# Kernel optimization log

Hardware: AMD Instinct MI355X
Metric: run time of the kernel (lower is better)

## Reference

```python
import jax, jax.numpy as jnp
import numpy as np
from jax.ops import segment_sum

N_NODES = 100000
N_EDGES = 3200000
NUM_FEATURES = 256


def setup_inputs() -> dict:
    key = jax.random.key(0)
    ks = jax.random.split(key, 12)
    def lin(k, fan_in, fan_out):
        bound = 1.0 / np.sqrt(fan_in)
        kw, kb = jax.random.split(k)
        W = jax.random.uniform(kw, (fan_in, fan_out), jnp.float32, -bound, bound)
        b = jax.random.uniform(kb, (fan_out,), jnp.float32, -bound, bound)
        return W, b
    x = jax.random.normal(ks[0], (N_NODES, NUM_FEATURES), jnp.float32)
    edge_index = jax.random.randint(ks[1], (2, N_EDGES), 0, N_NODES, jnp.int64 if jax.config.jax_enable_x64 else jnp.int32)
    W1, b1 = lin(ks[2], NUM_FEATURES, 64)
    W2, b2 = lin(ks[3], 64, 32)
    W3, b3 = lin(ks[4], 32, 16)
    Ws02, bs02 = lin(ks[5], NUM_FEATURES, 32)
    Ws03, bs03 = lin(ks[6], NUM_FEATURES, 16)
    Ws13, bs13 = lin(ks[7], 64, 16)
    Wout, bout = lin(ks[8], 16, 1)
    return dict(x=x, edge_index=edge_index, W1=W1, b1=b1, W2=W2, b2=b2,
                W3=W3, b3=b3, Ws02=Ws02, bs02=bs02, Ws03=Ws03, bs03=bs03,
                Ws13=Ws13, bs13=bs13, Wout=Wout, bout=bout)


def _deg_inv_sqrt(edge_index, n_nodes):
    # gcn_norm with self-loops: degree counted at target nodes, +1 for self-loop
    dst = edge_index[1]
    deg = segment_sum(jnp.ones(edge_index.shape[1], jnp.float32), dst, num_segments=n_nodes) + 1.0
    return jnp.where(deg > 0, jax.lax.rsqrt(deg), 0.0)


def _gcn_conv(x, W, b, edge_index, dinv):
    # PyG GCNConv: h = x W; out[i] = sum_{j->i} dinv[j]*dinv[i]*h[j] + dinv[i]^2*h[i] + b
    src, dst = edge_index[0], edge_index[1]
    h = x @ W                                   # [N, out]
    norm = (dinv[src] * dinv[dst])[:, None]     # [E, 1]
    agg = segment_sum(h[src] * norm, dst, num_segments=x.shape[0])
    agg = agg + (dinv * dinv)[:, None] * h      # self-loop term
    return agg + b


def reference(x, edge_index, W1, b1, W2, b2, W3, b3,
              Ws02, bs02, Ws03, bs03, Ws13, bs13, Wout, bout):
    # Dropout in eval mode (identity).
    dinv = _deg_inv_sqrt(edge_index, x.shape[0])
    x1 = jax.nn.relu(_gcn_conv(x, W1, b1, edge_index, dinv))
    x2 = jax.nn.relu(_gcn_conv(x1, W2, b2, edge_index, dinv) + x @ Ws02 + bs02)
    x3 = jax.nn.relu(_gcn_conv(x2, W3, b3, edge_index, dinv)
                     + x @ Ws03 + bs03 + x1 @ Ws13 + bs13)
    return jax.nn.sigmoid(x3 @ Wout + bout)
```

## Files before the change

kernel.cpp:

```cpp
#include <hip/hip_runtime.h>
#include <hip/hip_bf16.h>
#include <math.h>


#define NBUCK_MAX 512
#define P1_CHUNK 8192
#define EPT 32
#define BCAP 9216

typedef __attribute__((ext_vector_type(8))) short bfrag;
typedef __attribute__((ext_vector_type(4))) float f4_t;

__device__ inline float uaf(unsigned u) { return __uint_as_float(u); }
__device__ inline ushort f2bf(float f) {
    __hip_bfloat16 b = __float2bfloat16(f);
    return *reinterpret_cast<ushort*>(&b);
}
__device__ inline bfrag cvt8(const float4 a, const float4 b) {
    union { ushort u[8]; bfrag f; } r;
    r.u[0] = f2bf(a.x); r.u[1] = f2bf(a.y); r.u[2] = f2bf(a.z); r.u[3] = f2bf(a.w);
    r.u[4] = f2bf(b.x); r.u[5] = f2bf(b.y); r.u[6] = f2bf(b.z); r.u[7] = f2bf(b.w);
    return r.f;
}
__device__ inline bfrag ld_bfrag(const ushort* p) {
    const uint4 raw = *reinterpret_cast<const uint4*>(p);
    return *reinterpret_cast<const bfrag*>(&raw);
}


__global__ __launch_bounds__(256) void bucket_hist_kernel(
    const int* __restrict__ dst, int E, int* __restrict__ bucket_count, int nbuckets)
{
    __shared__ int lhist[NBUCK_MAX];
    for (int i = threadIdx.x; i < nbuckets; i += 256) lhist[i] = 0;
    __syncthreads();
    const int stride = gridDim.x * 256;
    for (int e = blockIdx.x * 256 + threadIdx.x; e < E; e += stride)
        atomicAdd(&lhist[dst[e] >> 8], 1);
    __syncthreads();
    for (int i = threadIdx.x; i < nbuckets; i += 256) {
        int c = lhist[i];
        if (c) atomicAdd(&bucket_count[i], c);
    }
}

__global__ __launch_bounds__(512) void bucket_scan_kernel(
    const int* __restrict__ bucket_count, int* __restrict__ bucket_base,
    int* __restrict__ bucket_cursor, int nbuckets)
{
    __shared__ int tmp[512];
    const int tid = threadIdx.x;
    int v = (tid < nbuckets) ? bucket_count[tid] : 0;
    tmp[tid] = v;
    __syncthreads();
    for (int off = 1; off < 512; off <<= 1) {
        int t = (tid >= off) ? tmp[tid - off] : 0;
        __syncthreads();
        tmp[tid] += t;
        __syncthreads();
    }
    if (tid < nbuckets) {
        int base = tmp[tid] - v;
        bucket_base[tid]   = base;
        bucket_cursor[tid] = base;
    }
}

__global__ __launch_bounds__(256) void partition_kernel(
    const int* __restrict__ src, const int* __restrict__ dst, int E,
    int* __restrict__ bucket_cursor, unsigned int* __restrict__ keys, int nbuckets)
{
    __shared__ int hist[NBUCK_MAX];
    __shared__ int lofs[NBUCK_MAX];
    __shared__ int gbase[NBUCK_MAX];
    __shared__ int lcur[NBUCK_MAX];
    __shared__ int ssum[256];
    __shared__ unsigned int stage[P1_CHUNK];
    __shared__ int gidx[P1_CHUNK];

    const int tid = threadIdx.x;
    const int e0  = blockIdx.x * P1_CHUNK;
    const int nE  = min(P1_CHUNK, E - e0);

    for (int i = tid; i < NBUCK_MAX; i += 256) { hist[i] = 0; lcur[i] = 0; }
    __syncthreads();

    int myb[EPT];
    unsigned int mypk[EPT];
#pragma unroll
    for (int j = 0; j < EPT; ++j) {
        const int e = e0 + tid + j * 256;
        if (e < E) {
            const int d = dst[e];
            myb[j]  = d >> 8;
            mypk[j] = ((unsigned int)(d & 255) << 17) | (unsigned int)src[e];
            atomicAdd(&hist[myb[j]], 1);
        } else myb[j] = -1;
    }
    __syncthreads();

    int a0 = (2 * tid     < nbuckets) ? hist[2 * tid]     : 0;
    int a1 = (2 * tid + 1 < nbuckets) ? hist[2 * tid + 1] : 0;
    ssum[tid] = a0 + a1;
    __syncthreads();
    for (int off = 1; off < 256; off <<= 1) {
        int t = (tid >= off) ? ssum[tid - off] : 0;
        __syncthreads();
        ssum[tid] += t;
        __syncthreads();
    }
    const int ex = ssum[tid] - (a0 + a1);
    if (2 * tid     < nbuckets) lofs[2 * tid]     = ex;
    if (2 * tid + 1 < nbuckets) lofs[2 * tid + 1] = ex + a0;
    __syncthreads();

    for (int i = tid; i < nbuckets; i += 256)
        gbase[i] = atomicAdd(&bucket_cursor[i], hist[i]);
    __syncthreads();

#pragma unroll
    for (int j = 0; j < EPT; ++j) {
        if (myb[j] >= 0) {
            const int b = myb[j];
            const int l = lofs[b] + atomicAdd(&lcur[b], 1);
            stage[l] = mypk[j];
            gidx[l]  = gbase[b] - lofs[b] + l;
        }
    }
    __syncthreads();

    for (int i = tid; i < nE; i += 256)
        keys[gidx[i]] = stage[i];
}

__global__ __launch_bounds__(256) void csr_build_kernel(
    const unsigned int* __restrict__ keys, const int* __restrict__ bucket_base,
    const int* __restrict__ bucket_count,
    int* __restrict__ row_off, float* __restrict__ dinv, int* __restrict__ col,
    int N, int E)
{
    __shared__ unsigned int inb[BCAP];
    __shared__ int outv[BCAP];
    __shared__ int hist[256];
    __shared__ int lofs[256];
    __shared__ int ssum[256];

    const int tid  = threadIdx.x;
    const int b    = blockIdx.x;
    const int base = bucket_base[b];
    const int cnt  = min(bucket_count[b], BCAP);
    const int n0   = b << 8;
    const int nn   = min(256, N - n0);

    for (int i = tid; i < cnt; i += 256) inb[i] = keys[base + i];
    hist[tid] = 0;
    __syncthreads();

    for (int i = tid; i < cnt; i += 256)
        atomicAdd(&hist[inb[i] >> 17], 1);
    __syncthreads();

    ssum[tid] = hist[tid];
    __syncthreads();
    for (int off = 1; off < 256; off <<= 1) {
        int t = (tid >= off) ? ssum[tid - off] : 0;
        __syncthreads();
        ssum[tid] += t;
        __syncthreads();
    }
    lofs[tid] = ssum[tid] - hist[tid];

    if (tid < nn) {
        row_off[n0 + tid] = base + lofs[tid];
        dinv[n0 + tid]    = rsqrtf((float)hist[tid] + 1.0f);
    }
    if (b == 0 && tid == 0) row_off[N] = E;
    __syncthreads();

    hist[tid] = 0;
    __syncthreads();

    for (int i = tid; i < cnt; i += 256) {
        const unsigned int k = inb[i];
        const int node = k >> 17;
        const int l = lofs[node] + atomicAdd(&hist[node], 1);
        outv[l] = (int)(k & 0x1FFFF);
    }
    __syncthreads();

    for (int i = tid; i < cnt; i += 256)
        col[base + i] = outv[i];
}


__global__ __launch_bounds__(256) void prep_weights_kernel(
    const float* __restrict__ W1, const float* __restrict__ Ws02,
    const float* __restrict__ Ws03, const float* __restrict__ W2,
    const float* __restrict__ Ws13, const float* __restrict__ W3,
    ushort* __restrict__ Wt0, ushort* __restrict__ Wt1, ushort* __restrict__ Wt2)
{
    int idx = blockIdx.x * 256 + threadIdx.x;
    if (idx < 32768) {
        int f = idx >> 8, k = idx & 255;
        float v = 0.f;
        if (f < 64)       v = W1[k * 64 + f];
        else if (f < 96)  v = Ws02[k * 32 + (f - 64)];
        else if (f < 112) v = Ws03[k * 16 + (f - 96)];
        Wt0[idx] = f2bf(v);
    } else if (idx < 32768 + 3072) {
        int t = idx - 32768;
        int f = t >> 6, k = t & 63;
        float v = (f < 32) ? W2[k * 32 + f] : Ws13[k * 16 + (f - 32)];
        Wt1[t] = f2bf(v);
    } else if (idx < 32768 + 3072 + 512) {
        int t = idx - 32768 - 3072;
        int f = t >> 5, k = t & 31;
        Wt2[t] = f2bf(W3[k * 16 + f]);
    }
}


__global__ __launch_bounds__(256, 2) void gemm_mfma0(
    const float* __restrict__ X, const ushort* __restrict__ Wt0,
    const float* __restrict__ bs02, const float* __restrict__ bs03,
    const float* __restrict__ dinv,
    __hip_bfloat16* __restrict__ g1, float* __restrict__ pre2,
    float* __restrict__ pre3, int N)
{
    __shared__ __align__(16) float Xs[64 * 256];

    const int tid  = threadIdx.x;
    const int lane = tid & 63;
    const int wf   = tid >> 6;
    const int n0   = blockIdx.x * 64;
    const int mrow = lane & 15;
    const int kq   = (lane >> 4) * 8;

    bfrag bfr[2][8];
#pragma unroll
    for (int ft = 0; ft < 2; ++ft) {
        const ushort* wr = &Wt0[(size_t)(wf * 32 + ft * 16 + mrow) * 256 + kq];
#pragma unroll
        for (int p = 0; p < 8; ++p)
            bfr[ft][p] = ld_bfrag(&wr[p * 32]);
    }

    {
        for (int i = 0; i < 16; ++i) {
            const int lrow = wf * 16 + i;
            const int grow = min(n0 + lrow, N - 1);
            const float* gsrc = X + (size_t)grow * 256 +
                                (size_t)((lane ^ (lrow & 7)) * 4);
            __builtin_amdgcn_global_load_lds(
                (const __attribute__((address_space(1))) unsigned int*)gsrc,
                (__attribute__((address_space(3))) unsigned int*)&Xs[lrow * 256],
                16, 0, 0);
        }
    }
    __syncthreads();

    f4_t acc[4][2];
#pragma unroll
    for (int a = 0; a < 4; ++a)
#pragma unroll
        for (int b = 0; b < 2; ++b) acc[a][b] = {0.f, 0.f, 0.f, 0.f};

    const float4* Xs4 = reinterpret_cast<const float4*>(Xs);

#pragma unroll
    for (int p = 0; p < 8; ++p) {
        bfrag af[4];
#pragma unroll
        for (int mt = 0; mt < 4; ++mt) {
            const int r  = mt * 16 + mrow;
            const int c0 = p * 8 + (lane >> 4) * 2;
            const float4 u0 = Xs4[r * 64 + (c0 ^ (r & 7))];
            const float4 u1 = Xs4[r * 64 + ((c0 + 1) ^ (r & 7))];
            af[mt] = cvt8(u0, u1);
        }
#pragma unroll
        for (int mt = 0; mt < 4; ++mt)
#pragma unroll
            for (int ft = 0; ft < 2; ++ft)
                acc[mt][ft] = __builtin_amdgcn_mfma_f32_16x16x32_bf16(
                    af[mt], bfr[ft][p], acc[mt][ft], 0, 0, 0);
    }

#pragma unroll
    for (int mt = 0; mt < 4; ++mt) {
#pragma unroll
        for (int ft = 0; ft < 2; ++ft) {
            const int fg = wf * 32 + ft * 16 + mrow;
#pragma unroll
            for (int r = 0; r < 4; ++r) {
                const int n = n0 + mt * 16 + (lane >> 4) * 4 + r;
                if (n >= N) continue;
                const float a = acc[mt][ft][r];
                if (fg < 64) {
                    g1[(size_t)n * 64 + fg] = __float2bfloat16(dinv[n] * a);
                } else if (fg < 96) {
                    pre2[(size_t)n * 32 + (fg - 64)] = a + bs02[fg - 64];
                } else if (fg < 112) {
                    pre3[(size_t)n * 16 + (fg - 96)] = a + bs03[fg - 96];
                }
            }
        }
    }
}

__global__ __launch_bounds__(256) void gemm_mfma1(
    const ushort* __restrict__ X1, const ushort* __restrict__ Wt1,
    const float* __restrict__ bs13, const float* __restrict__ dinv,
    __hip_bfloat16* __restrict__ g2, float* __restrict__ pre3, int N)
{
    const int tid  = threadIdx.x;
    const int lane = tid & 63;
    const int wave = tid >> 6;
    const int n0   = blockIdx.x * 128 + wave * 32;
    const int mrow = lane & 15;
    const int kq   = (lane >> 4) * 8;

    f4_t acc[2][3];
#pragma unroll
    for (int a = 0; a < 2; ++a)
#pragma unroll
        for (int b = 0; b < 3; ++b) acc[a][b] = {0.f, 0.f, 0.f, 0.f};

    const ushort* xrow[2];
#pragma unroll
    for (int mt = 0; mt < 2; ++mt) {
        int r = n0 + mt * 16 + mrow;
        r = (r < N) ? r : (N - 1);
        xrow[mt] = &X1[(size_t)r * 64 + kq];
    }
    const ushort* wrow[3];
#pragma unroll
    for (int ft = 0; ft < 3; ++ft)
        wrow[ft] = &Wt1[(size_t)(ft * 16 + mrow) * 64 + kq];

#pragma unroll
    for (int p = 0; p < 2; ++p) {
        bfrag af[2], bf[3];
#pragma unroll
        for (int mt = 0; mt < 2; ++mt) af[mt] = ld_bfrag(&xrow[mt][p * 32]);
#pragma unroll
        for (int ft = 0; ft < 3; ++ft) bf[ft] = ld_bfrag(&wrow[ft][p * 32]);
#pragma unroll
        for (int mt = 0; mt < 2; ++mt)
#pragma unroll
            for (int ft = 0; ft < 3; ++ft)
                acc[mt][ft] = __builtin_amdgcn_mfma_f32_16x16x32_bf16(
                    af[mt], bf[ft], acc[mt][ft], 0, 0, 0);
    }

#pragma unroll
    for (int mt = 0; mt < 2; ++mt) {
#pragma unroll
        for (int ft = 0; ft < 3; ++ft) {
            const int fg = ft * 16 + mrow;
#pragma unroll
            for (int r = 0; r < 4; ++r) {
                const int n = n0 + mt * 16 + (lane >> 4) * 4 + r;
                if (n >= N) continue;
                const float a = acc[mt][ft][r];
                if (fg < 32) {
                    g2[(size_t)n * 32 + fg] = __float2bfloat16(dinv[n] * a);
                } else {
                    pre3[(size_t)n * 16 + (fg - 32)] += a + bs13[fg - 32];
                }
            }
        }
    }
}

__global__ __launch_bounds__(256) void gemm_mfma2(
    const ushort* __restrict__ X2, const ushort* __restrict__ Wt2,
    const float* __restrict__ dinv, __hip_bfloat16* __restrict__ g3, int N)
{
    const int tid  = threadIdx.x;
    const int lane = tid & 63;
    const int wave = tid >> 6;
    const int n0   = blockIdx.x * 128 + wave * 32;
    const int mrow = lane & 15;
    const int kq   = (lane >> 4) * 8;

    f4_t acc[2];
#pragma unroll
    for (int a = 0; a < 2; ++a) acc[a] = {0.f, 0.f, 0.f, 0.f};

    const bfrag bf = ld_bfrag(&Wt2[(size_t)mrow * 32 + kq]);
#pragma unroll
    for (int mt = 0; mt < 2; ++mt) {
        int r = n0 + mt * 16 + mrow;
        r = (r < N) ? r : (N - 1);
        const bfrag af = ld_bfrag(&X2[(size_t)r * 32 + kq]);
        acc[mt] = __builtin_amdgcn_mfma_f32_16x16x32_bf16(af, bf, acc[mt], 0, 0, 0);
    }

#pragma unroll
    for (int mt = 0; mt < 2; ++mt) {
#pragma unroll
        for (int r = 0; r < 4; ++r) {
            const int n = n0 + mt * 16 + (lane >> 4) * 4 + r;
            if (n >= N) continue;
            g3[(size_t)n * 16 + mrow] = __float2bfloat16(dinv[n] * acc[mt][r]);
        }
    }
}


template<int F, int MODE>
__global__ __launch_bounds__(256) void agg_kernel(
    const ushort* __restrict__ g, const float* __restrict__ dinv,
    const int* __restrict__ row_off, const int* __restrict__ col,
    const float* __restrict__ bias, const float* __restrict__ pre,
    const float* __restrict__ Wout, const float* __restrict__ bout,
    void* __restrict__ out, int N)
{
    constexpr int FG  = F / 4;
    constexpr int EPW = 64 / FG;
    constexpr int U   = (F == 64) ? 8 : (F == 32 ? 4 : 2);

    const int lane = threadIdx.x & 63;
    const int wv   = threadIdx.x >> 6;
    const int i    = blockIdx.x * 4 + wv;
    if (i >= N) return;

    const int fg = lane % FG;
    const int eo = lane / FG;
    const int fb = fg * 4;

    float a0 = 0.f, a1 = 0.f, a2 = 0.f, a3 = 0.f;
    const int s = row_off[i], e = row_off[i + 1];
    for (int p = s + eo; p < e; p += U * EPW) {
        int js[U];
        float m[U];
#pragma unroll
        for (int u = 0; u < U; ++u) {
            const int q = p + u * EPW;
            m[u]  = (q < e) ? 1.0f : 0.0f;
            js[u] = col[min(q, e - 1)];
        }
        uint2 w[U];
#pragma unroll
        for (int u = 0; u < U; ++u)
            w[u] = *reinterpret_cast<const uint2*>(&g[(size_t)js[u] * F + fb]);
#pragma unroll
        for (int u = 0; u < U; ++u) {
            a0 = fmaf(m[u], uaf(w[u].x << 16),         a0);
            a1 = fmaf(m[u], uaf(w[u].x & 0xffff0000u), a1);
            a2 = fmaf(m[u], uaf(w[u].y << 16),         a2);
            a3 = fmaf(m[u], uaf(w[u].y & 0xffff0000u), a3);
        }
    }
#pragma unroll
    for (int off = FG; off < 64; off <<= 1) {
        a0 += __shfl_xor(a0, off);
        a1 += __shfl_xor(a1, off);
        a2 += __shfl_xor(a2, off);
        a3 += __shfl_xor(a3, off);
    }

    const uint2 ws = *reinterpret_cast<const uint2*>(&g[(size_t)i * F + fb]);
    const float di = dinv[i];
    float v0 = di * (a0 + uaf(ws.x << 16))         + bias[fb + 0];
    float v1 = di * (a1 + uaf(ws.x & 0xffff0000u)) + bias[fb + 1];
    float v2 = di * (a2 + uaf(ws.y << 16))         + bias[fb + 2];
    float v3 = di * (a3 + uaf(ws.y & 0xffff0000u)) + bias[fb + 3];
    if (MODE != 0) {
        const float4 pv = *reinterpret_cast<const float4*>(&pre[(size_t)i * F + fb]);
        v0 += pv.x; v1 += pv.y; v2 += pv.z; v3 += pv.w;
    }
    v0 = fmaxf(v0, 0.f); v1 = fmaxf(v1, 0.f);
    v2 = fmaxf(v2, 0.f); v3 = fmaxf(v3, 0.f);

    if (MODE != 2) {
        if (lane < FG) {
            uint2 o;
            o.x = (unsigned)f2bf(v0) | ((unsigned)f2bf(v1) << 16);
            o.y = (unsigned)f2bf(v2) | ((unsigned)f2bf(v3) << 16);
            *reinterpret_cast<uint2*>(&((ushort*)out)[(size_t)i * F + fb]) = o;
        }
    } else {
        float t = v0 * Wout[fb] + v1 * Wout[fb + 1] +
                  v2 * Wout[fb + 2] + v3 * Wout[fb + 3];
        t += __shfl_xor(t, 1);
        t += __shfl_xor(t, 2);
        if (lane == 0)
            ((float*)out)[i] = 1.0f / (1.0f + expf(-(t + bout[0])));
    }
}


extern "C" void kernel_launch(void* const* d_in, const int* in_sizes, int n_in,
                              void* d_out, int out_size, void* d_ws, size_t ws_size,
                              hipStream_t stream)
{
    const float* x    = (const float*)d_in[0];
    const int*   edge = (const int*)d_in[1];
    const float* W1   = (const float*)d_in[2];
    const float* b1   = (const float*)d_in[3];
    const float* W2   = (const float*)d_in[4];
    const float* b2   = (const float*)d_in[5];
    const float* W3   = (const float*)d_in[6];
    const float* b3   = (const float*)d_in[7];
    const float* Ws02 = (const float*)d_in[8];
    const float* bs02 = (const float*)d_in[9];
    const float* Ws03 = (const float*)d_in[10];
    const float* bs03 = (const float*)d_in[11];
    const float* Ws13 = (const float*)d_in[12];
    const float* bs13 = (const float*)d_in[13];
    const float* Wout = (const float*)d_in[14];
    const float* bout = (const float*)d_in[15];

    const int N = in_sizes[0] / 256;
    const int E = in_sizes[1] / 2;
    const int* srcv = edge;
    const int* dstv = edge + E;
    const int nbuckets = (N + 255) >> 8;

    char* ws = (char*)d_ws;
    size_t off = 0;
    auto alloc = [&](size_t bytes) -> void* {
        void* p = ws + off;
        off += (bytes + 255) & ~(size_t)255;
        return p;
    };
    unsigned int* keys = (unsigned int*)alloc((size_t)E * 4);
    int*   col      = (int*)  alloc((size_t)E * 4);
    int*   bcount   = (int*)  alloc((size_t)NBUCK_MAX * 4);
    int*   bbase    = (int*)  alloc((size_t)NBUCK_MAX * 4);
    int*   bcursor  = (int*)  alloc((size_t)NBUCK_MAX * 4);
    int*   row_off  = (int*)  alloc((size_t)(N + 1) * 4);
    float* dinv     = (float*)alloc((size_t)N * 4);
    ushort* Wt0     = (ushort*)alloc((size_t)128 * 256 * 2);
    ushort* Wt1     = (ushort*)alloc((size_t)48 * 64 * 2);
    ushort* Wt2     = (ushort*)alloc((size_t)16 * 32 * 2);
    ushort* g1      = (ushort*)alloc((size_t)N * 64 * 2);
    ushort* x1      = (ushort*)alloc((size_t)N * 64 * 2);
    ushort* g2      = (ushort*)alloc((size_t)N * 32 * 2);
    ushort* x2      = (ushort*)alloc((size_t)N * 32 * 2);
    ushort* g3      = (ushort*)alloc((size_t)N * 16 * 2);
    float* pre2     = (float*)alloc((size_t)N * 32 * 4);
    float* pre3     = (float*)alloc((size_t)N * 16 * 4);

    prep_weights_kernel<<<142, 256, 0, stream>>>(W1, Ws02, Ws03, W2, Ws13, W3,
                                                 Wt0, Wt1, Wt2);
    hipMemsetAsync(bcount, 0, (size_t)NBUCK_MAX * 4, stream);
    bucket_hist_kernel<<<1024, 256, 0, stream>>>(dstv, E, bcount, nbuckets);
    bucket_scan_kernel<<<1, 512, 0, stream>>>(bcount, bbase, bcursor, nbuckets);
    partition_kernel<<<(E + P1_CHUNK - 1) / P1_CHUNK, 256, 0, stream>>>(
        srcv, dstv, E, bcursor, keys, nbuckets);
    csr_build_kernel<<<nbuckets, 256, 0, stream>>>(
        keys, bbase, bcount, row_off, dinv, col, N, E);

    const int ab = (N + 3) / 4;

    gemm_mfma0<<<(N + 63) / 64, 256, 0, stream>>>(
        x, Wt0, bs02, bs03, dinv, (__hip_bfloat16*)g1, pre2, pre3, N);
    agg_kernel<64, 0><<<ab, 256, 0, stream>>>(g1, dinv, row_off, col,
                                              b1, nullptr, nullptr, nullptr, x1, N);
    gemm_mfma1<<<(N + 127) / 128, 256, 0, stream>>>(
        x1, Wt1, bs13, dinv, (__hip_bfloat16*)g2, pre3, N);
    agg_kernel<32, 1><<<ab, 256, 0, stream>>>(g2, dinv, row_off, col,
                                              b2, pre2, nullptr, nullptr, x2, N);
    gemm_mfma2<<<(N + 127) / 128, 256, 0, stream>>>(
        x2, Wt2, dinv, (__hip_bfloat16*)g3, N);
    agg_kernel<16, 2><<<ab, 256, 0, stream>>>(g3, dinv, row_off, col,
                                              b3, pre3, Wout, bout, d_out, N);
}
```

Baseline: 442.5 us.

## Double-buffer X staging in gemm0 and stage GEMM outputs through LDS for coalesced stores

gemm_mfma0 now loads X in four 64-column chunks into a two-slot LDS buffer, prefetching the next chunk while MFMAs run on the current one. This cuts LDS use from 64KB to 32KB so occupancy can rise to 3 blocks per CU. All three GEMM kernels now write their outputs to LDS first and then store them to global memory with 16-byte vector writes, replacing scattered 2- and 4-byte stores. The cost is extra barriers and a shared-memory round trip in each kernel.

```diff
diff --git a/kernel.cpp b/kernel.cpp
--- a/kernel.cpp
+++ b/kernel.cpp
@@ -220,21 +220,22 @@
 }
 
 
-__global__ __launch_bounds__(256, 2) void gemm_mfma0(
+__global__ __launch_bounds__(256, 3) void gemm_mfma0(
     const float* __restrict__ X, const ushort* __restrict__ Wt0,
     const float* __restrict__ bs02, const float* __restrict__ bs03,
     const float* __restrict__ dinv,
     __hip_bfloat16* __restrict__ g1, float* __restrict__ pre2,
     float* __restrict__ pre3, int N)
 {
-    __shared__ __align__(16) float Xs[64 * 256];
+    __shared__ __align__(16) float Xs[2][64 * 64];
 
     const int tid  = threadIdx.x;
     const int lane = tid & 63;
     const int wf   = tid >> 6;
     const int n0   = blockIdx.x * 64;
     const int mrow = lane & 15;
-    const int kq   = (lane >> 4) * 8;
+    const int q    = lane >> 4;
+    const int kq   = q * 8;
 
     bfrag bfr[2][8];
 #pragma unroll
@@ -245,19 +246,26 @@
             bfr[ft][p] = ld_bfrag(&wr[p * 32]);
     }
 
-    {
-        for (int i = 0; i < 16; ++i) {
-            const int lrow = wf * 16 + i;
-            const int grow = min(n0 + lrow, N - 1);
-            const float* gsrc = X + (size_t)grow * 256 +
-                                (size_t)((lane ^ (lrow & 7)) * 4);
+    int srow[4], schunk[4];
+#pragma unroll
+    for (int j = 0; j < 4; ++j) {
+        const int R = wf * 16 + j * 4 + q;
+        srow[j]   = min(n0 + R, N - 1);
+        schunk[j] = mrow ^ (R & 7);
+    }
+
+    auto STAGE = [&](int buf, int kc) {
+#pragma unroll
+        for (int j = 0; j < 4; ++j) {
+            const float* gsrc =
+                X + (size_t)srow[j] * 256 + kc * 64 + schunk[j] * 4;
             __builtin_amdgcn_global_load_lds(
                 (const __attribute__((address_space(1))) unsigned int*)gsrc,
-                (__attribute__((address_space(3))) unsigned int*)&Xs[lrow * 256],
+                (__attribute__((address_space(3))) unsigned int*)
+                    &Xs[buf][(wf * 16 + j * 4) * 64],
                 16, 0, 0);
         }
-    }
-    __syncthreads();
+    };
 
     f4_t acc[4][2];
 #pragma unroll
@@ -265,46 +273,96 @@
 #pragma unroll
         for (int b = 0; b < 2; ++b) acc[a][b] = {0.f, 0.f, 0.f, 0.f};
 
-    const float4* Xs4 = reinterpret_cast<const float4*>(Xs);
-
-#pragma unroll
-    for (int p = 0; p < 8; ++p) {
-        bfrag af[4];
+    STAGE(0, 0);
+    __syncthreads();
+
+    int cur = 0;
+    for (int kc = 0; kc < 4; ++kc) {
+        if (kc < 3) STAGE(cur ^ 1, kc + 1);
+        const float4* Xs4 = reinterpret_cast<const float4*>(Xs[cur]);
+#pragma unroll
+        for (int pl = 0; pl < 2; ++pl) {
+            bfrag af[4];
+#pragma unroll
+            for (int mt = 0; mt < 4; ++mt) {
+                const int r  = mt * 16 + mrow;
+                const int c0 = pl * 8 + q * 2;
+                const float4 u0 = Xs4[r * 16 + (c0 ^ (r & 7))];
+                const float4 u1 = Xs4[r * 16 + ((c0 + 1) ^ (r & 7))];
+                af[mt] = cvt8(u0, u1);
+            }
+            const int pg = kc * 2 + pl;
+#pragma unroll
+            for (int mt = 0; mt < 4; ++mt)
+#pragma unroll
+                for (int ft = 0; ft < 2; ++ft)
+                    acc[mt][ft] = __builtin_amdgcn_mfma_f32_16x16x32_bf16(
+                        af[mt], bfr[ft][pg], acc[mt][ft], 0, 0, 0);
+        }
+        __syncthreads();
+        cur ^= 1;
+    }
+
+    char* sm = (char*)Xs;
+    ushort* g1s = (ushort*)sm;
+    float*  p2s = (float*)(sm + 8192);
+    float*  p3s = (float*)(sm + 16384);
+
+    if (wf < 2) {
 #pragma unroll
         for (int mt = 0; mt < 4; ++mt) {
-            const int r  = mt * 16 + mrow;
-            const int c0 = p * 8 + (lane >> 4) * 2;
-            const float4 u0 = Xs4[r * 64 + (c0 ^ (r & 7))];
-            const float4 u1 = Xs4[r * 64 + ((c0 + 1) ^ (r & 7))];
-            af[mt] = cvt8(u0, u1);
-        }
+#pragma unroll
+            for (int r = 0; r < 4; ++r) {
+                const int nl = mt * 16 + q * 4 + r;
+                const float di = dinv[min(n0 + nl, N - 1)];
+#pragma unroll
+                for (int ft = 0; ft < 2; ++ft)
+                    g1s[nl * 64 + wf * 32 + ft * 16 + mrow] =
+                        f2bf(di * acc[mt][ft][r]);
+            }
+        }
+    } else if (wf == 2) {
 #pragma unroll
         for (int mt = 0; mt < 4; ++mt)
 #pragma unroll
             for (int ft = 0; ft < 2; ++ft)
-                acc[mt][ft] = __builtin_amdgcn_mfma_f32_16x16x32_bf16(
-                    af[mt], bfr[ft][p], acc[mt][ft], 0, 0, 0);
-    }
-
-#pragma unroll
-    for (int mt = 0; mt < 4; ++mt) {
-#pragma unroll
-        for (int ft = 0; ft < 2; ++ft) {
-            const int fg = wf * 32 + ft * 16 + mrow;
-#pragma unroll
-            for (int r = 0; r < 4; ++r) {
-                const int n = n0 + mt * 16 + (lane >> 4) * 4 + r;
-                if (n >= N) continue;
-                const float a = acc[mt][ft][r];
-                if (fg < 64) {
-                    g1[(size_t)n * 64 + fg] = __float2bfloat16(dinv[n] * a);
-                } else if (fg < 96) {
-                    pre2[(size_t)n * 32 + (fg - 64)] = a + bs02[fg - 64];
-                } else if (fg < 112) {
-                    pre3[(size_t)n * 16 + (fg - 96)] = a + bs03[fg - 96];
-                }
-            }
-        }
+#pragma unroll
+                for (int r = 0; r < 4; ++r)
+                    p2s[(mt * 16 + q * 4 + r) * 32 + ft * 16 + mrow] =
+                        acc[mt][ft][r] + bs02[ft * 16 + mrow];
+    } else {
+#pragma unroll
+        for (int mt = 0; mt < 4; ++mt)
+#pragma unroll
+            for (int r = 0; r < 4; ++r)
+                p3s[(mt * 16 + q * 4 + r) * 16 + mrow] =
+                    acc[mt][0][r] + bs03[mrow];
+    }
+    __syncthreads();
+
+    const uint4* g1v = (const uint4*)g1s;
+    const uint4* p2v = (const uint4*)p2s;
+    const uint4* p3v = (const uint4*)p3s;
+#pragma unroll
+    for (int t = 0; t < 2; ++t) {
+        const int i   = t * 256 + tid;
+        const int row = i >> 3;
+        if (n0 + row < N)
+            *(uint4*)((ushort*)g1 + (size_t)(n0 + row) * 64 + (i & 7) * 8) =
+                g1v[i];
+    }
+#pragma unroll
+    for (int t = 0; t < 2; ++t) {
+        const int i   = t * 256 + tid;
+        const int row = i >> 3;
+        if (n0 + row < N)
+            *(uint4*)(pre2 + (size_t)(n0 + row) * 32 + (i & 7) * 4) = p2v[i];
+    }
+    {
+        const int i   = tid;
+        const int row = i >> 2;
+        if (n0 + row < N)
+            *(uint4*)(pre3 + (size_t)(n0 + row) * 16 + (i & 3) * 4) = p3v[i];
     }
 }
 
@@ -313,12 +371,17 @@
     const float* __restrict__ bs13, const float* __restrict__ dinv,
     __hip_bfloat16* __restrict__ g2, float* __restrict__ pre3, int N)
 {
+    __shared__ __align__(16) ushort g2s[128 * 32];
+    __shared__ __align__(16) float  p3s[128 * 16];
+
     const int tid  = threadIdx.x;
     const int lane = tid & 63;
     const int wave = tid >> 6;
-    const int n0   = blockIdx.x * 128 + wave * 32;
+    const int nb   = blockIdx.x * 128;
+    const int n0   = nb + wave * 32;
     const int mrow = lane & 15;
-    const int kq   = (lane >> 4) * 8;
+    const int q    = lane >> 4;
+    const int kq   = q * 8;
 
     f4_t acc[2][3];
 #pragma unroll
@@ -356,19 +419,37 @@
 #pragma unroll
     for (int mt = 0; mt < 2; ++mt) {
 #pragma unroll
-        for (int ft = 0; ft < 3; ++ft) {
-            const int fg = ft * 16 + mrow;
-#pragma unroll
-            for (int r = 0; r < 4; ++r) {
-                const int n = n0 + mt * 16 + (lane >> 4) * 4 + r;
-                if (n >= N) continue;
-                const float a = acc[mt][ft][r];
-                if (fg < 32) {
-                    g2[(size_t)n * 32 + fg] = __float2bfloat16(dinv[n] * a);
-                } else {
-                    pre3[(size_t)n * 16 + (fg - 32)] += a + bs13[fg - 32];
-                }
-            }
+        for (int r = 0; r < 4; ++r) {
+            const int nl = wave * 32 + mt * 16 + q * 4 + r;
+            const float di = dinv[min(nb + nl, N - 1)];
+            g2s[nl * 32 +      mrow] = f2bf(di * acc[mt][0][r]);
+            g2s[nl * 32 + 16 + mrow] = f2bf(di * acc[mt][1][r]);
+            p3s[nl * 16 + mrow] = acc[mt][2][r] + bs13[mrow];
+        }
+    }
+    __syncthreads();
+
+    const uint4*  g2v = (const uint4*)g2s;
+    const float4* p3v = (const float4*)p3s;
+#pragma unroll
+    for (int t = 0; t < 2; ++t) {
+        const int i   = t * 256 + tid;
+        const int row = i >> 2;
+        if (nb + row < N)
+            *(uint4*)((ushort*)g2 + (size_t)(nb + row) * 32 + (i & 3) * 8) =
+                g2v[i];
+    }
+#pragma unroll
+    for (int t = 0; t < 2; ++t) {
+        const int i   = t * 256 + tid;
+        const int row = i >> 2;
+        if (nb + row < N) {
+            float4* dst =
+                (float4*)(pre3 + (size_t)(nb + row) * 16 + (i & 3) * 4);
+            float4 v = *dst;
+            const float4 s = p3v[i];
+            v.x += s.x; v.y += s.y; v.z += s.z; v.w += s.w;
+            *dst = v;
         }
     }
 }
@@ -377,12 +458,16 @@
     const ushort* __restrict__ X2, const ushort* __restrict__ Wt2,
     const float* __restrict__ dinv, __hip_bfloat16* __restrict__ g3, int N)
 {
+    __shared__ __align__(16) ushort g3s[128 * 16];
+
     const int tid  = threadIdx.x;
     const int lane = tid & 63;
     const int wave = tid >> 6;
-    const int n0   = blockIdx.x * 128 + wave * 32;
+    const int nb   = blockIdx.x * 128;
+    const int n0   = nb + wave * 32;
     const int mrow = lane & 15;
-    const int kq   = (lane >> 4) * 8;
+    const int q    = lane >> 4;
+    const int kq   = q * 8;
 
     f4_t acc[2];
 #pragma unroll
@@ -401,10 +486,20 @@
     for (int mt = 0; mt < 2; ++mt) {
 #pragma unroll
         for (int r = 0; r < 4; ++r) {
-            const int n = n0 + mt * 16 + (lane >> 4) * 4 + r;
-            if (n >= N) continue;
-            g3[(size_t)n * 16 + mrow] = __float2bfloat16(dinv[n] * acc[mt][r]);
-        }
+            const int nl = wave * 32 + mt * 16 + q * 4 + r;
+            const float di = dinv[min(nb + nl, N - 1)];
+            g3s[nl * 16 + mrow] = f2bf(di * acc[mt][r]);
+        }
+    }
+    __syncthreads();
+
+    const uint4* g3v = (const uint4*)g3s;
+    {
+        const int i   = tid;
+        const int row = i >> 1;
+        if (nb + row < N)
+            *(uint4*)((ushort*)g3 + (size_t)(nb + row) * 16 + (i & 1) * 8) =
+                g3v[i];
     }
 }
 
```

Result: faster. 427.0 us (-3.5%).
